# Kernel tuning notes

Hardware: AMD Instinct MI355X
Metric: run time of the kernel (lower is better)

## Reference

```python
import jax, jax.numpy as jnp
import numpy as np

OUT_CHANNELS = 16
PH = PW = 7          # output_size
SR = 2               # sampling_ratio


def setup_inputs() -> dict:
    key = jax.random.key(0)
    k1, k2, k3, k4 = jax.random.split(key, 4)
    B, C, H, W = 4, OUT_CHANNELS * PH * PW, 80, 80
    feat = jax.random.normal(k1, (B, C, H, W), dtype=jnp.float32)
    N = 512
    bidx = jax.random.randint(k2, (N,), 0, B).astype(jnp.float32)
    tl = jax.random.uniform(k3, (N, 2), minval=0.0, maxval=0.7)   # x1, y1 (normalized)
    sz = jax.random.uniform(k4, (N, 2), minval=0.05, maxval=0.3)  # box size
    rois = jnp.concatenate([bidx[:, None], tl, tl + sz], axis=1)  # [N,5]
    return {"input": feat, "rois": rois}


def _psroi_one(feat_ps, roi):
    # feat_ps: [B, Co, PH, PW, H, W]  (position-sensitive channel layout)
    B, Co, _, _, H, W = feat_ps.shape
    f = feat_ps[roi[0].astype(jnp.int32)]              # [Co, PH, PW, H, W]
    x1 = roi[1] * W; y1 = roi[2] * H
    x2 = roi[3] * W; y2 = roi[4] * H                   # adaptive spatial_scale = (H, W)
    roi_h = jnp.maximum(y2 - y1, 0.1)
    roi_w = jnp.maximum(x2 - x1, 0.1)
    bin_h = roi_h / PH
    bin_w = roi_w / PW
    # sample coordinates per bin: [PH,SR] and [PW,SR]
    ys = y1 + jnp.arange(PH, dtype=f.dtype)[:, None] * bin_h + (jnp.arange(SR, dtype=f.dtype)[None, :] + 0.5) * bin_h / SR
    xs = x1 + jnp.arange(PW, dtype=f.dtype)[:, None] * bin_w + (jnp.arange(SR, dtype=f.dtype)[None, :] + 0.5) * bin_w / SR
    ym = (ys >= -1.0) & (ys <= H)
    xm = (xs >= -1.0) & (xs <= W)
    yc = jnp.clip(ys, 0.0, H - 1)
    xc = jnp.clip(xs, 0.0, W - 1)
    y0 = jnp.floor(yc).astype(jnp.int32)
    x0 = jnp.floor(xc).astype(jnp.int32)
    y1i = jnp.minimum(y0 + 1, H - 1)
    x1i = jnp.minimum(x0 + 1, W - 1)
    ly = yc - y0.astype(f.dtype); hy = 1.0 - ly        # [PH,SR]
    lx = xc - x0.astype(f.dtype); hx = 1.0 - lx        # [PW,SR]
    I = jnp.arange(PH)[:, None, None, None]            # bin row index
    J = jnp.arange(PW)[None, None, :, None]            # bin col index

    def g(Y, X):
        # gather f[c, i, j, Y[i,sy], X[j,sx]] -> [Co, PH, SR, PW, SR]
        return f[:, I, J, Y[:, :, None, None], X[None, None, :, :]]

    v = (g(y0, x0)  * (hy[:, :, None, None] * hx[None, None])
       + g(y0, x1i) * (hy[:, :, None, None] * lx[None, None])
       + g(y1i, x0) * (ly[:, :, None, None] * hx[None, None])
       + g(y1i, x1i) * (ly[:, :, None, None] * lx[None, None]))
    v = v * (ym[:, :, None, None] & xm[None, None]).astype(v.dtype)
    return v.mean(axis=(2, 4))                          # [Co, PH, PW]


def reference(input, rois):
    B, C, H, W = input.shape
    feat_ps = input.reshape(B, OUT_CHANNELS, PH, PW, H, W)
    rois = rois.reshape(-1, 5)
    out = jax.vmap(lambda r: _psroi_one(feat_ps, r))(rois)  # [N, Co, PH, PW]
    return out
```

## Files before the change

### kernel.cpp

```cpp
#include <hip/hip_runtime.h>

#define NB   4
#define CO   16
#define PH   7
#define PW   7
#define SR   2
#define HH   80
#define WW   80
#define NROI 512
#define CIJ  (CO*PH*PW)
#define PLANE (HH*WW)
#define NF4  (PLANE/4)

typedef float f4v __attribute__((ext_vector_type(4), aligned(16)));

#define WS_ORDER_OFF 64
#define WS_GEOM_OFF  2048

__global__ __launch_bounds__(512) void psroi_prep_kernel(
    const float* __restrict__ rois, int* __restrict__ base,
    unsigned short* __restrict__ order, f4v* __restrict__ geom)
{
    __shared__ int cnt[NB];
    __shared__ int cbase[NB + 1];
    int n = threadIdx.x;
    if (n < NB) cnt[n] = 0;
    __syncthreads();
    int b = (int)rois[n * 5 + 0];
    int rank = atomicAdd(&cnt[b], 1);
    __syncthreads();
    if (n == 0) {
        cbase[0] = 0;
        for (int k = 0; k < NB; ++k) cbase[k + 1] = cbase[k] + cnt[k];
        for (int k = 0; k <= NB; ++k) base[k] = cbase[k];
    }
    __syncthreads();
    int pos = cbase[b] + rank;
    order[pos] = (unsigned short)n;

    float x1 = rois[n * 5 + 1] * (float)WW;
    float y1 = rois[n * 5 + 2] * (float)HH;
    float x2 = rois[n * 5 + 3] * (float)WW;
    float y2 = rois[n * 5 + 4] * (float)HH;
    f4v g;
    g.x = x1;
    g.y = y1;
    g.z = fmaxf(x2 - x1, 0.1f) * (1.0f / PW);
    g.w = fmaxf(y2 - y1, 0.1f) * (1.0f / PH);
    geom[pos] = g;
}

__global__ __launch_bounds__(256) void psroi_main_kernel(
    const float* __restrict__ feat,
    const int* __restrict__ base,
    const unsigned short* __restrict__ order,
    const f4v* __restrict__ geom,
    float* __restrict__ out)
{
    __shared__ __align__(16) float sp[PLANE];

    int u   = blockIdx.x;
    int cij = u >> 2;
    int b   = u & 3;
    int rem = cij % (PH * PW);
    int i = rem / PW;
    int j = rem % PW;
    int n = threadIdx.x;

    const f4v* src = (const f4v*)(feat + ((size_t)b * CIJ + (size_t)cij) * PLANE);
    f4v* dst = (f4v*)sp;
    #pragma unroll
    for (int it = 0; it < 6; ++it)
        dst[it * 256 + n] = src[it * 256 + n];
    {
        int e = 1536 + n;
        if (e < NF4) dst[e] = src[e];
    }

    int lo = base[b];
    int hi = base[b + 1];

    __syncthreads();

    for (int t = lo + n; t < hi; t += 256) {
        int m = (int)order[t];
        f4v g = geom[t];
        float x1 = g.x, y1 = g.y, bin_w = g.z, bin_h = g.w;

        float acc = 0.0f;
        #pragma unroll
        for (int sy = 0; sy < SR; ++sy) {
            float ys = y1 + (float)i * bin_h + ((float)sy + 0.5f) * bin_h / (float)SR;
            bool ymask = (ys >= -1.0f) && (ys <= (float)HH);
            float yc = fminf(fmaxf(ys, 0.0f), (float)(HH - 1));
            int   y0 = (int)floorf(yc);
            int   y1i = min(y0 + 1, HH - 1);
            float ly = yc - (float)y0, hy = 1.0f - ly;
            #pragma unroll
            for (int sx = 0; sx < SR; ++sx) {
                float xs = x1 + (float)j * bin_w + ((float)sx + 0.5f) * bin_w / (float)SR;
                bool xmask = (xs >= -1.0f) && (xs <= (float)WW);
                float xc = fminf(fmaxf(xs, 0.0f), (float)(WW - 1));
                int   x0 = (int)floorf(xc);
                int   x0c = min(x0, WW - 2);
                bool  sh = (x0 != x0c);
                float lx = xc - (float)x0, hx = 1.0f - lx;

                float t0 = sp[y0  * WW + x0c], t1 = sp[y0  * WW + x0c + 1];
                float b0 = sp[y1i * WW + x0c], b1 = sp[y1i * WW + x0c + 1];

                float v00 = sh ? t1 : t0;
                float v10 = sh ? b1 : b0;
                float v = (v00 * hx + t1 * lx) * hy + (v10 * hx + b1 * lx) * ly;
                if (ymask && xmask) acc += v;
            }
        }
        out[(size_t)m * CIJ + cij] = acc * 0.25f;
    }
}

extern "C" void kernel_launch(void* const* d_in, const int* in_sizes, int n_in,
                              void* d_out, int out_size, void* d_ws, size_t ws_size,
                              hipStream_t stream)
{
    const float* feat = (const float*)d_in[0];
    const float* rois = (const float*)d_in[1];
    float* out = (float*)d_out;

    char* ws = (char*)d_ws;
    int* base = (int*)ws;
    unsigned short* order = (unsigned short*)(ws + WS_ORDER_OFF);
    f4v* geom = (f4v*)(ws + WS_GEOM_OFF);

    psroi_prep_kernel<<<1, NROI, 0, stream>>>(rois, base, order, geom);
    psroi_main_kernel<<<CIJ * NB, 256, 0, stream>>>(feat, base, order, geom, out);
}
```

Measured before the change: 111.3 us.

## Load feature plane via global_load_lds and split sample rows across lane pairs

Replaces the register-staged copy of each feature plane into shared memory with direct global-to-LDS loads, so the data no longer passes through VGPRs. It also gives each ROI to two lanes, one per vertical sample row, and combines their partial sums with a lane shuffle. This roughly doubles how many threads are busy per ROI batch, since each batch has only about 128 ROIs. The cost is an extra shuffle, and the direct-LDS load must be synchronised correctly before the barrier.

```diff
diff --git a/kernel.cpp b/kernel.cpp
--- a/kernel.cpp
+++ b/kernel.cpp
@@ -13,6 +13,9 @@
 #define NF4  (PLANE/4)
 
 typedef float f4v __attribute__((ext_vector_type(4), aligned(16)));
+
+typedef __attribute__((address_space(1))) const void gvoid_t;
+typedef __attribute__((address_space(3))) void svoid_t;
 
 #define WS_ORDER_OFF 64
 #define WS_GEOM_OFF  2048
@@ -68,13 +71,17 @@
     int n = threadIdx.x;
 
     const f4v* src = (const f4v*)(feat + ((size_t)b * CIJ + (size_t)cij) * PLANE);
-    f4v* dst = (f4v*)sp;
+    int wbase = n & ~63;
     #pragma unroll
-    for (int it = 0; it < 6; ++it)
-        dst[it * 256 + n] = src[it * 256 + n];
-    {
-        int e = 1536 + n;
-        if (e < NF4) dst[e] = src[e];
+    for (int it = 0; it < 6; ++it) {
+        const f4v* g = src + it * 256 + n;
+        float* l = sp + (size_t)(it * 256 + wbase) * 4;
+        __builtin_amdgcn_global_load_lds((gvoid_t*)g, (svoid_t*)l, 16, 0, 0);
+    }
+    if (n < 64) {
+        const f4v* g = src + 1536 + n;
+        float* l = sp + (size_t)1536 * 4;
+        __builtin_amdgcn_global_load_lds((gvoid_t*)g, (svoid_t*)l, 16, 0, 0);
     }
 
     int lo = base[b];
@@ -82,40 +89,44 @@
 
     __syncthreads();
 
-    for (int t = lo + n; t < hi; t += 256) {
+    int sy = n & 1;
+    float sy_off = ((float)sy + 0.5f) * (1.0f / SR);
+
+    for (int t = lo + (n >> 1); t < hi; t += 128) {
         int m = (int)order[t];
         f4v g = geom[t];
         float x1 = g.x, y1 = g.y, bin_w = g.z, bin_h = g.w;
 
-        float acc = 0.0f;
+        float ys = y1 + ((float)i + sy_off) * bin_h;
+        bool ymask = (ys >= -1.0f) && (ys <= (float)HH);
+        float yc = fminf(fmaxf(ys, 0.0f), (float)(HH - 1));
+        int   y0 = (int)floorf(yc);
+        int   y1i = min(y0 + 1, HH - 1);
+        float ly = yc - (float)y0, hy = 1.0f - ly;
+
+        float partial = 0.0f;
         #pragma unroll
-        for (int sy = 0; sy < SR; ++sy) {
-            float ys = y1 + (float)i * bin_h + ((float)sy + 0.5f) * bin_h / (float)SR;
-            bool ymask = (ys >= -1.0f) && (ys <= (float)HH);
-            float yc = fminf(fmaxf(ys, 0.0f), (float)(HH - 1));
-            int   y0 = (int)floorf(yc);
-            int   y1i = min(y0 + 1, HH - 1);
-            float ly = yc - (float)y0, hy = 1.0f - ly;
-            #pragma unroll
-            for (int sx = 0; sx < SR; ++sx) {
-                float xs = x1 + (float)j * bin_w + ((float)sx + 0.5f) * bin_w / (float)SR;
-                bool xmask = (xs >= -1.0f) && (xs <= (float)WW);
-                float xc = fminf(fmaxf(xs, 0.0f), (float)(WW - 1));
-                int   x0 = (int)floorf(xc);
-                int   x0c = min(x0, WW - 2);
-                bool  sh = (x0 != x0c);
-                float lx = xc - (float)x0, hx = 1.0f - lx;
+        for (int sx = 0; sx < SR; ++sx) {
+            float xs = x1 + ((float)j + ((float)sx + 0.5f) * (1.0f / SR)) * bin_w;
+            bool xmask = (xs >= -1.0f) && (xs <= (float)WW);
+            float xc = fminf(fmaxf(xs, 0.0f), (float)(WW - 1));
+            int   x0 = (int)floorf(xc);
+            int   x0c = min(x0, WW - 2);
+            bool  sh = (x0 != x0c);
+            float lx = xc - (float)x0, hx = 1.0f - lx;
 
-                float t0 = sp[y0  * WW + x0c], t1 = sp[y0  * WW + x0c + 1];
-                float b0 = sp[y1i * WW + x0c], b1 = sp[y1i * WW + x0c + 1];
+            float t0 = sp[y0  * WW + x0c], t1 = sp[y0  * WW + x0c + 1];
+            float b0 = sp[y1i * WW + x0c], b1 = sp[y1i * WW + x0c + 1];
 
-                float v00 = sh ? t1 : t0;
-                float v10 = sh ? b1 : b0;
-                float v = (v00 * hx + t1 * lx) * hy + (v10 * hx + b1 * lx) * ly;
-                if (ymask && xmask) acc += v;
-            }
+            float v00 = sh ? t1 : t0;
+            float v10 = sh ? b1 : b0;
+            float v = (v00 * hx + t1 * lx) * hy + (v10 * hx + b1 * lx) * ly;
+            if (ymask && xmask) partial += v;
         }
-        out[(size_t)m * CIJ + cij] = acc * 0.25f;
+
+        float other = __shfl_xor(partial, 1);
+        if (sy == 0)
+            out[(size_t)m * CIJ + cij] = (partial + other) * 0.25f;
     }
 }
 
```

Result: no change. 111.8 us (+0.5%).
